# Kernel tuning notes

Measured on AMD Instinct MI355X. Metric: run time of the kernel, lower is better.

## Reference

```python
import jax, jax.numpy as jnp
import numpy as np

VOCAB = 65      # char-level vocab (tiny-shakespeare)
N_EMBED = 32    # hardcoded global in source
BLOCK = 8       # block_size
N_HEADS = 4
HEAD_SIZE = N_EMBED // N_HEADS  # 8
B = 131072


def setup_inputs() -> dict:
    key = jax.random.key(0)
    ks = jax.random.split(key, 10)
    s = 0.02
    return {
        "idx": jax.random.randint(ks[0], (B, BLOCK), 0, VOCAB),
        "tok_emb": jax.random.normal(ks[1], (VOCAB, N_EMBED), jnp.float32) * s,
        "pos_emb": jax.random.normal(ks[2], (BLOCK, N_EMBED), jnp.float32) * s,
        # per-head projections stacked: [H, n_embed, head_size]
        "Wq": jax.random.normal(ks[3], (N_HEADS, N_EMBED, HEAD_SIZE), jnp.float32) * s,
        "Wk": jax.random.normal(ks[4], (N_HEADS, N_EMBED, HEAD_SIZE), jnp.float32) * s,
        "Wv": jax.random.normal(ks[5], (N_HEADS, N_EMBED, HEAD_SIZE), jnp.float32) * s,
        "Wf": jax.random.normal(ks[6], (N_EMBED, N_EMBED), jnp.float32) * s,
        "bf": jnp.zeros((N_EMBED,), jnp.float32),
        "Wl": jax.random.normal(ks[7], (N_EMBED, VOCAB), jnp.float32) * s,
        "bl": jnp.zeros((VOCAB,), jnp.float32),
    }


def reference(idx, tok_emb, pos_emb, Wq, Wk, Wv, Wf, bf, Wl, bl):
    B_, T = idx.shape
    x = tok_emb[idx] + pos_emb[:T]                      # [B,T,C]
    q = jnp.einsum('btc,hcd->bhtd', x, Wq)              # [B,H,T,hs]
    k = jnp.einsum('btc,hcd->bhtd', x, Wk)
    v = jnp.einsum('btc,hcd->bhtd', x, Wv)
    # NOTE: original scales by n_embed**-0.5 (C of input x), not head_size
    wei = jnp.einsum('btd,bhsd->bhts'.replace('btd', 'bhtd'), q, k) * (N_EMBED ** -0.5)
    causal = jnp.tril(jnp.ones((T, T), bool))
    wei = jnp.where(causal, wei, -jnp.inf)
    wei = jax.nn.softmax(wei, axis=-1)
    out = jnp.einsum('bhts,bhsd->bhtd', wei, v)         # [B,H,T,hs]
    # concat heads along feature dim (head h -> slice [h*hs:(h+1)*hs])
    x = out.transpose(0, 2, 1, 3).reshape(B_, T, N_EMBED)
    x = jax.nn.relu(x @ Wf + bf)                        # FeedForward (no residual)
    logits = x @ Wl + bl                                # [B,T,VOCAB]
    return logits
```

## Files before the change

### kernel.cpp

```cpp
#include <hip/hip_runtime.h>

#define VOCAB   65
#define NEMB    32
#define TBLK    8
#define NHEAD   4
#define HS      8
#define NB      131072

#define TABSZ   16640
#define WFB_OFF (3 * TABSZ)
#define WLB_OFF (3 * TABSZ + 512)

typedef _Float16 f16x8 __attribute__((ext_vector_type(8)));
typedef float    f32x4 __attribute__((ext_vector_type(4)));

__global__ void build_tables(const float* __restrict__ tok_emb,
                             const float* __restrict__ pos_emb,
                             const float* __restrict__ Wq,
                             const float* __restrict__ Wk,
                             const float* __restrict__ Wv,
                             const float* __restrict__ Wf,
                             const float* __restrict__ Wl,
                             float* __restrict__ ws) {
    int e = blockIdx.x * blockDim.x + threadIdx.x;
    if (e < 3 * TABSZ) {
        int tab = e / TABSZ;
        int r   = e % TABSZ;
        int t   = r / (VOCAB * NEMB);
        int rem = r % (VOCAB * NEMB);
        int tok = rem / NEMB;
        int hd  = rem % NEMB;
        int h = hd >> 3, d = hd & 7;
        const float* W = (tab == 0) ? Wq : (tab == 1 ? Wk : Wv);
        float acc = 0.f;
        #pragma unroll
        for (int c = 0; c < NEMB; ++c) {
            float x = tok_emb[tok * NEMB + c] + pos_emb[t * NEMB + c];
            acc = fmaf(x, W[(h * NEMB + c) * HS + d], acc);
        }
        ws[tab * TABSZ + r] = acc;
    } else if (e < 3 * TABSZ + 1024) {
        int i = e - 3 * TABSZ;
        int j = i >> 5, c = i & 31;
        ((_Float16*)(ws + WFB_OFF))[i] = (_Float16)Wf[c * NEMB + j];
    } else if (e < 3 * TABSZ + 1024 + 2560) {
        int i = e - (3 * TABSZ + 1024);
        int j = i >> 5, c = i & 31;
        ((_Float16*)(ws + WLB_OFF))[i] =
            (_Float16)((j < VOCAB) ? Wl[c * VOCAB + j] : 0.f);
    }
}

__global__ __launch_bounds__(256, 4) void fused_lm(
        const int*   __restrict__ idx,
        const float* __restrict__ ws,
        const float* __restrict__ bfv,
        const float* __restrict__ blv,
        float*       __restrict__ out) {

    __shared__ int      sidx[256];
    __shared__ _Float16 Abuf[256][40];
    __shared__ float    lbuf[4][1040];

    const float* Qtab = ws;
    const float* Ktab = ws + TABSZ;
    const float* Vtab = ws + 2 * TABSZ;
    const _Float16* wfb = (const _Float16*)(ws + WFB_OFF);
    const _Float16* wlb = (const _Float16*)(ws + WLB_OFF);

    const int tid  = threadIdx.x;
    const int row0 = blockIdx.x * 256;

    sidx[tid] = idx[row0 + tid];
    __syncthreads();

    const int b_loc = tid >> 3;
    const int t     = tid & 7;

    const int tok_t = sidx[tid];
    float4 q[8];
    {
        const float4* qrow = (const float4*)(Qtab + (t * VOCAB + tok_t) * NEMB);
        #pragma unroll
        for (int i = 0; i < 8; ++i) q[i] = qrow[i];
    }

    const float scale = 0.17677669529663687f;
    float wei[4][8];
    #pragma unroll
    for (int s = 0; s < 8; ++s) {
        const int toks = sidx[(b_loc << 3) | s];
        const float4* krow = (const float4*)(Ktab + (s * VOCAB + toks) * NEMB);
        #pragma unroll
        for (int h = 0; h < 4; ++h) {
            float4 ka = krow[2 * h], kb = krow[2 * h + 1];
            float4 qa = q[2 * h],    qb = q[2 * h + 1];
            float d = qa.x * ka.x + qa.y * ka.y + qa.z * ka.z + qa.w * ka.w
                    + qb.x * kb.x + qb.y * kb.y + qb.z * kb.z + qb.w * kb.w;
            wei[h][s] = (s <= t) ? d * scale : -__builtin_inff();
        }
    }

    #pragma unroll
    for (int h = 0; h < 4; ++h) {
        float m = wei[h][0];
        #pragma unroll
        for (int s = 1; s < 8; ++s) m = fmaxf(m, wei[h][s]);
        float sum = 0.f;
        #pragma unroll
        for (int s = 0; s < 8; ++s) {
            float e = __expf(wei[h][s] - m);
            wei[h][s] = e;
            sum += e;
        }
        float inv = 1.f / sum;
        #pragma unroll
        for (int s = 0; s < 8; ++s) wei[h][s] *= inv;
    }

    float xatt[32];
    #pragma unroll
    for (int i = 0; i < 32; ++i) xatt[i] = 0.f;
    #pragma unroll
    for (int s = 0; s < 8; ++s) {
        const int toks = sidx[(b_loc << 3) | s];
        const float4* vrow = (const float4*)(Vtab + (s * VOCAB + toks) * NEMB);
        #pragma unroll
        for (int h = 0; h < 4; ++h) {
            float4 va = vrow[2 * h], vb = vrow[2 * h + 1];
            float p = wei[h][s];
            xatt[h * 8 + 0] = fmaf(p, va.x, xatt[h * 8 + 0]);
            xatt[h * 8 + 1] = fmaf(p, va.y, xatt[h * 8 + 1]);
            xatt[h * 8 + 2] = fmaf(p, va.z, xatt[h * 8 + 2]);
            xatt[h * 8 + 3] = fmaf(p, va.w, xatt[h * 8 + 3]);
            xatt[h * 8 + 4] = fmaf(p, vb.x, xatt[h * 8 + 4]);
            xatt[h * 8 + 5] = fmaf(p, vb.y, xatt[h * 8 + 5]);
            xatt[h * 8 + 6] = fmaf(p, vb.z, xatt[h * 8 + 6]);
            xatt[h * 8 + 7] = fmaf(p, vb.w, xatt[h * 8 + 7]);
        }
    }

    {
        f16x8* arow = (f16x8*)&Abuf[tid][0];
        #pragma unroll
        for (int qd = 0; qd < 4; ++qd) {
            f16x8 v;
            #pragma unroll
            for (int e2 = 0; e2 < 8; ++e2) v[e2] = (_Float16)xatt[qd * 8 + e2];
            arow[qd] = v;
        }
    }
    __syncthreads();

    const int l  = tid & 63;
    const int w  = tid >> 6;
    const int lr = l & 15;
    const int lg = l >> 4;

    f16x8 afr[4];
    #pragma unroll
    for (int rt = 0; rt < 4; ++rt)
        afr[rt] = *(const f16x8*)&Abuf[w * 64 + rt * 16 + lr][lg * 8];

    f16x8 bwf0 = *(const f16x8*)&wfb[(0 * 16 + lr) * 32 + lg * 8];
    f16x8 bwf1 = *(const f16x8*)&wfb[(1 * 16 + lr) * 32 + lg * 8];
    const float bias0 = bfv[lr], bias1 = bfv[16 + lr];

    #pragma unroll
    for (int rt = 0; rt < 4; ++rt) {
        f32x4 a0 = {0.f, 0.f, 0.f, 0.f}, a1 = {0.f, 0.f, 0.f, 0.f};
        a0 = __builtin_amdgcn_mfma_f32_16x16x32_f16(afr[rt], bwf0, a0, 0, 0, 0);
        a1 = __builtin_amdgcn_mfma_f32_16x16x32_f16(afr[rt], bwf1, a1, 0, 0, 0);
        #pragma unroll
        for (int j = 0; j < 4; ++j) {
            int row = w * 64 + rt * 16 + lg * 4 + j;
            Abuf[row][lr]      = (_Float16)fmaxf(a0[j] + bias0, 0.f);
            Abuf[row][16 + lr] = (_Float16)fmaxf(a1[j] + bias1, 0.f);
        }
    }
    __syncthreads();

    f16x8 ffr[4];
    #pragma unroll
    for (int rt = 0; rt < 4; ++rt)
        ffr[rt] = *(const f16x8*)&Abuf[w * 64 + rt * 16 + lr][lg * 8];

    f16x8 bwl[5];
    float lbias[5];
    #pragma unroll
    for (int ct = 0; ct < 5; ++ct) {
        bwl[ct] = *(const f16x8*)&wlb[(ct * 16 + lr) * 32 + lg * 8];
        int col = ct * 16 + lr;
        lbias[ct] = (col < VOCAB) ? blv[col] : 0.f;
    }

    const size_t blockBase = (size_t)blockIdx.x * (256 * VOCAB);
    float* lb = lbuf[w];

    for (int rt = 0; rt < 4; ++rt) {
        #pragma unroll
        for (int ct = 0; ct < 5; ++ct) {
            f32x4 acc = {0.f, 0.f, 0.f, 0.f};
            acc = __builtin_amdgcn_mfma_f32_16x16x32_f16(ffr[rt], bwl[ct], acc, 0, 0, 0);
            int col = ct * 16 + lr;
            if (col < VOCAB) {
                #pragma unroll
                for (int j = 0; j < 4; ++j)
                    lb[(lg * 4 + j) * VOCAB + col] = acc[j] + lbias[ct];
            }
        }
        __syncthreads();

        const size_t outBase = blockBase + (size_t)(w * 64 + rt * 16) * VOCAB;
        #pragma unroll
        for (int i = 0; i < 4; ++i) {
            int p = i * 64 + l;
            f32x4 v4 = *(const f32x4*)&lb[p * 4];
            *(f32x4*)&out[outBase + p * 4] = v4;
        }
        if (l < 4) {
            int p = 256 + l;
            f32x4 v4 = *(const f32x4*)&lb[p * 4];
            *(f32x4*)&out[outBase + p * 4] = v4;
        }
        __syncthreads();
    }
}

extern "C" void kernel_launch(void* const* d_in, const int* in_sizes, int n_in,
                              void* d_out, int out_size, void* d_ws, size_t ws_size,
                              hipStream_t stream) {
    const int*   idx     = (const int*)  d_in[0];
    const float* tok_emb = (const float*)d_in[1];
    const float* pos_emb = (const float*)d_in[2];
    const float* Wq      = (const float*)d_in[3];
    const float* Wk      = (const float*)d_in[4];
    const float* Wv      = (const float*)d_in[5];
    const float* Wf      = (const float*)d_in[6];
    const float* bf      = (const float*)d_in[7];
    const float* Wl      = (const float*)d_in[8];
    const float* bl      = (const float*)d_in[9];
    float* ws  = (float*)d_ws;
    float* out = (float*)d_out;

    hipLaunchKernelGGL(build_tables, dim3(209), dim3(256), 0, stream,
                       tok_emb, pos_emb, Wq, Wk, Wv, Wf, Wl, ws);
    hipLaunchKernelGGL(fused_lm, dim3(4096), dim3(256), 0, stream,
                       idx, ws, bf, bl, out);
}
```

Before: 387.5 us.

## Precompute exp attention score table and replace block barriers with wave fences

Adds a build kernel that precomputes exp(q·k*scale) per head for every (t, tok_t, s, tok_s) combination, about 270K entries of 4 floats. The main kernel then gathers one 16-byte entry per key position instead of computing dot products and the max-subtraction softmax. Block-wide __syncthreads are replaced by wave-local lgkmcnt fences, relying on each wave only touching its own LDS rows. Risks are larger scattered gathers from a ~4MB table, skipping max subtraction (safe only while scores stay small), and a fallback path used when the workspace is too small.

New measurement: 375.2 us. -3.2%, faster.

```diff
diff --git a/kernel.cpp b/kernel.cpp
--- a/kernel.cpp
+++ b/kernel.cpp
@@ -2,17 +2,24 @@
 
 #define VOCAB   65
 #define NEMB    32
-#define TBLK    8
 #define NHEAD   4
 #define HS      8
-#define NB      131072
-
-#define TABSZ   16640
-#define WFB_OFF (3 * TABSZ)
-#define WLB_OFF (3 * TABSZ + 512)
+
+#define TABSZ    16640
+#define WFB_OFF  (3 * TABSZ)
+#define WLB_OFF  (3 * TABSZ + 512)
+#define ETAB_OFF (3 * TABSZ + 512 + 1280)
+#define ETAB_N   (8 * VOCAB * 8 * VOCAB)
+#define NEED_WS_BYTES ((size_t)(ETAB_OFF + 4 * ETAB_N) * 4)
 
 typedef _Float16 f16x8 __attribute__((ext_vector_type(8)));
 typedef float    f32x4 __attribute__((ext_vector_type(4)));
+
+__device__ __forceinline__ void wave_fence() {
+    __builtin_amdgcn_sched_barrier(0);
+    asm volatile("s_waitcnt lgkmcnt(0)" ::: "memory");
+    __builtin_amdgcn_sched_barrier(0);
+}
 
 __global__ void build_tables(const float* __restrict__ tok_emb,
                              const float* __restrict__ pos_emb,
@@ -51,6 +58,29 @@
     }
 }
 
+__global__ void build_etab(float* __restrict__ ws) {
+    int e = blockIdx.x * blockDim.x + threadIdx.x;
+    if (e >= ETAB_N) return;
+    int tok_s = e % VOCAB;
+    int s     = (e / VOCAB) & 7;
+    int tok_t = (e / (VOCAB * 8)) % VOCAB;
+    int t     =  e / (VOCAB * 8 * VOCAB);
+    const float* qrow = ws + (t * VOCAB + tok_t) * NEMB;
+    const float* krow = ws + TABSZ + (s * VOCAB + tok_s) * NEMB;
+    const float scale = 0.17677669529663687f;
+    f32x4 r;
+    #pragma unroll
+    for (int h = 0; h < 4; ++h) {
+        float d = 0.f;
+        #pragma unroll
+        for (int dd = 0; dd < 8; ++dd)
+            d = fmaf(qrow[h * 8 + dd], krow[h * 8 + dd], d);
+        r[h] = expf(d * scale);
+    }
+    ((f32x4*)(ws + ETAB_OFF))[e] = r;
+}
+
+template<bool ETAB>
 __global__ __launch_bounds__(256, 4) void fused_lm(
         const int*   __restrict__ idx,
         const float* __restrict__ ws,
@@ -62,8 +92,6 @@
     __shared__ _Float16 Abuf[256][40];
     __shared__ float    lbuf[4][1040];
 
-    const float* Qtab = ws;
-    const float* Ktab = ws + TABSZ;
     const float* Vtab = ws + 2 * TABSZ;
     const _Float16* wfb = (const _Float16*)(ws + WFB_OFF);
     const _Float16* wlb = (const _Float16*)(ws + WLB_OFF);
@@ -72,50 +100,72 @@
     const int row0 = blockIdx.x * 256;
 
     sidx[tid] = idx[row0 + tid];
-    __syncthreads();
+    wave_fence();
 
     const int b_loc = tid >> 3;
     const int t     = tid & 7;
-
     const int tok_t = sidx[tid];
-    float4 q[8];
-    {
+
+    float p[4][8];
+
+    if constexpr (ETAB) {
+        const float* Etab = ws + ETAB_OFF;
+        #pragma unroll
+        for (int s = 0; s < 8; ++s) {
+            const int toks = sidx[(b_loc << 3) | s];
+            const f32x4 ev = *(const f32x4*)(
+                Etab + (size_t)((((t * VOCAB + tok_t) * 8 + s) * VOCAB + toks)) * 4);
+            const bool ok = (s <= t);
+            #pragma unroll
+            for (int h = 0; h < 4; ++h) p[h][s] = ok ? ev[h] : 0.f;
+        }
+        #pragma unroll
+        for (int h = 0; h < 4; ++h) {
+            float sum = p[h][0];
+            #pragma unroll
+            for (int s = 1; s < 8; ++s) sum += p[h][s];
+            float inv = 1.f / sum;
+            #pragma unroll
+            for (int s = 0; s < 8; ++s) p[h][s] *= inv;
+        }
+    } else {
+        const float* Qtab = ws;
+        const float* Ktab = ws + TABSZ;
+        float4 q[8];
         const float4* qrow = (const float4*)(Qtab + (t * VOCAB + tok_t) * NEMB);
         #pragma unroll
         for (int i = 0; i < 8; ++i) q[i] = qrow[i];
-    }
-
-    const float scale = 0.17677669529663687f;
-    float wei[4][8];
-    #pragma unroll
-    for (int s = 0; s < 8; ++s) {
-        const int toks = sidx[(b_loc << 3) | s];
-        const float4* krow = (const float4*)(Ktab + (s * VOCAB + toks) * NEMB);
+
+        const float scale = 0.17677669529663687f;
+        #pragma unroll
+        for (int s = 0; s < 8; ++s) {
+            const int toks = sidx[(b_loc << 3) | s];
+            const float4* krow = (const float4*)(Ktab + (s * VOCAB + toks) * NEMB);
+            #pragma unroll
+            for (int h = 0; h < 4; ++h) {
+                float4 ka = krow[2 * h], kb = krow[2 * h + 1];
+                float4 qa = q[2 * h],    qb = q[2 * h + 1];
+                float d = qa.x * ka.x + qa.y * ka.y + qa.z * ka.z + qa.w * ka.w
+                        + qb.x * kb.x + qb.y * kb.y + qb.z * kb.z + qb.w * kb.w;
+                p[h][s] = (s <= t) ? d * scale : -__builtin_inff();
+            }
+        }
         #pragma unroll
         for (int h = 0; h < 4; ++h) {
-            float4 ka = krow[2 * h], kb = krow[2 * h + 1];
-            float4 qa = q[2 * h],    qb = q[2 * h + 1];
-            float d = qa.x * ka.x + qa.y * ka.y + qa.z * ka.z + qa.w * ka.w
-                    + qb.x * kb.x + qb.y * kb.y + qb.z * kb.z + qb.w * kb.w;
-            wei[h][s] = (s <= t) ? d * scale : -__builtin_inff();
-        }
-    }
-
-    #pragma unroll
-    for (int h = 0; h < 4; ++h) {
-        float m = wei[h][0];
-        #pragma unroll
-        for (int s = 1; s < 8; ++s) m = fmaxf(m, wei[h][s]);
-        float sum = 0.f;
-        #pragma unroll
-        for (int s = 0; s < 8; ++s) {
-            float e = __expf(wei[h][s] - m);
-            wei[h][s] = e;
-            sum += e;
-        }
-        float inv = 1.f / sum;
-        #pragma unroll
-        for (int s = 0; s < 8; ++s) wei[h][s] *= inv;
+            float m = p[h][0];
+            #pragma unroll
+            for (int s = 1; s < 8; ++s) m = fmaxf(m, p[h][s]);
+            float sum = 0.f;
+            #pragma unroll
+            for (int s = 0; s < 8; ++s) {
+                float e = __expf(p[h][s] - m);
+                p[h][s] = e;
+                sum += e;
+            }
+            float inv = 1.f / sum;
+            #pragma unroll
+            for (int s = 0; s < 8; ++s) p[h][s] *= inv;
+        }
     }
 
     float xatt[32];
@@ -128,15 +178,15 @@
         #pragma unroll
         for (int h = 0; h < 4; ++h) {
             float4 va = vrow[2 * h], vb = vrow[2 * h + 1];
-            float p = wei[h][s];
-            xatt[h * 8 + 0] = fmaf(p, va.x, xatt[h * 8 + 0]);
-            xatt[h * 8 + 1] = fmaf(p, va.y, xatt[h * 8 + 1]);
-            xatt[h * 8 + 2] = fmaf(p, va.z, xatt[h * 8 + 2]);
-            xatt[h * 8 + 3] = fmaf(p, va.w, xatt[h * 8 + 3]);
-            xatt[h * 8 + 4] = fmaf(p, vb.x, xatt[h * 8 + 4]);
-            xatt[h * 8 + 5] = fmaf(p, vb.y, xatt[h * 8 + 5]);
-            xatt[h * 8 + 6] = fmaf(p, vb.z, xatt[h * 8 + 6]);
-            xatt[h * 8 + 7] = fmaf(p, vb.w, xatt[h * 8 + 7]);
+            float pp = p[h][s];
+            xatt[h * 8 + 0] = fmaf(pp, va.x, xatt[h * 8 + 0]);
+            xatt[h * 8 + 1] = fmaf(pp, va.y, xatt[h * 8 + 1]);
+            xatt[h * 8 + 2] = fmaf(pp, va.z, xatt[h * 8 + 2]);
+            xatt[h * 8 + 3] = fmaf(pp, va.w, xatt[h * 8 + 3]);
+            xatt[h * 8 + 4] = fmaf(pp, vb.x, xatt[h * 8 + 4]);
+            xatt[h * 8 + 5] = fmaf(pp, vb.y, xatt[h * 8 + 5]);
+            xatt[h * 8 + 6] = fmaf(pp, vb.z, xatt[h * 8 + 6]);
+            xatt[h * 8 + 7] = fmaf(pp, vb.w, xatt[h * 8 + 7]);
         }
     }
 
@@ -150,7 +200,7 @@
             arow[qd] = v;
         }
     }
-    __syncthreads();
+    wave_fence();
 
     const int l  = tid & 63;
     const int w  = tid >> 6;
@@ -178,7 +228,7 @@
             Abuf[row][16 + lr] = (_Float16)fmaxf(a1[j] + bias1, 0.f);
         }
     }
-    __syncthreads();
+    wave_fence();
 
     f16x8 ffr[4];
     #pragma unroll
@@ -209,21 +259,21 @@
                     lb[(lg * 4 + j) * VOCAB + col] = acc[j] + lbias[ct];
             }
         }
-        __syncthreads();
+        wave_fence();
 
         const size_t outBase = blockBase + (size_t)(w * 64 + rt * 16) * VOCAB;
         #pragma unroll
         for (int i = 0; i < 4; ++i) {
-            int p = i * 64 + l;
-            f32x4 v4 = *(const f32x4*)&lb[p * 4];
-            *(f32x4*)&out[outBase + p * 4] = v4;
+            int pidx = i * 64 + l;
+            f32x4 v4 = *(const f32x4*)&lb[pidx * 4];
+            *(f32x4*)&out[outBase + pidx * 4] = v4;
         }
         if (l < 4) {
-            int p = 256 + l;
-            f32x4 v4 = *(const f32x4*)&lb[p * 4];
-            *(f32x4*)&out[outBase + p * 4] = v4;
-        }
-        __syncthreads();
+            int pidx = 256 + l;
+            f32x4 v4 = *(const f32x4*)&lb[pidx * 4];
+            *(f32x4*)&out[outBase + pidx * 4] = v4;
+        }
+        wave_fence();
     }
 }
 
@@ -245,6 +295,13 @@
 
     hipLaunchKernelGGL(build_tables, dim3(209), dim3(256), 0, stream,
                        tok_emb, pos_emb, Wq, Wk, Wv, Wf, Wl, ws);
-    hipLaunchKernelGGL(fused_lm, dim3(4096), dim3(256), 0, stream,
-                       idx, ws, bf, bl, out);
-}
+
+    if (ws_size >= NEED_WS_BYTES) {
+        hipLaunchKernelGGL(build_etab, dim3(1057), dim3(256), 0, stream, ws);
+        hipLaunchKernelGGL(fused_lm<true>, dim3(4096), dim3(256), 0, stream,
+                           idx, ws, bf, bl, out);
+    } else {
+        hipLaunchKernelGGL(fused_lm<false>, dim3(4096), dim3(256), 0, stream,
+                           idx, ws, bf, bl, out);
+    }
+}
```
